# Kernel optimization log

Measured on AMD Instinct MI355X. Metric: run time of the kernel, lower is better.

Reference implementation:

```python
import jax, jax.numpy as jnp
import numpy as np

INPUT_SIZE = 256
HIDDEN_SIZE = 256
BATCH = 64
SEQ_LEN = 2048


def setup_inputs() -> dict:
    key = jax.random.key(0)
    ks = jax.random.split(key, 5)
    s_ih = 1.0 / np.sqrt(HIDDEN_SIZE)
    x = jax.random.normal(ks[0], (BATCH, SEQ_LEN, INPUT_SIZE), dtype=jnp.float32)
    W_ih = jax.random.uniform(ks[1], (4 * HIDDEN_SIZE, INPUT_SIZE), minval=-s_ih, maxval=s_ih, dtype=jnp.float32)
    W_hh = jax.random.uniform(ks[2], (4 * HIDDEN_SIZE, HIDDEN_SIZE), minval=-s_ih, maxval=s_ih, dtype=jnp.float32)
    b_ih = jax.random.uniform(ks[3], (4 * HIDDEN_SIZE,), minval=-s_ih, maxval=s_ih, dtype=jnp.float32)
    b_hh = jax.random.uniform(ks[4], (4 * HIDDEN_SIZE,), minval=-s_ih, maxval=s_ih, dtype=jnp.float32)
    return {"x": x, "W_ih": W_ih, "W_hh": W_hh, "b_ih": b_ih, "b_hh": b_hh}


def _lstm_forward(x, W_ih, W_hh, b_ih, b_hh):
    B, S, _ = x.shape
    H = W_hh.shape[1]
    # Precompute input projections for all timesteps in one big GEMM: [B,S,4H]
    x_proj = jnp.einsum('bsi,gi->bsg', x, W_ih) + b_ih + b_hh

    def step(carry, xp_t):
        h, c = carry
        gates = xp_t + h @ W_hh.T  # [B, 4H]
        i, f, g, o = jnp.split(gates, 4, axis=-1)
        i = jax.nn.sigmoid(i)
        f = jax.nn.sigmoid(f)
        g = jnp.tanh(g)
        o = jax.nn.sigmoid(o)
        c = f * c + i * g
        h = o * jnp.tanh(c)
        return (h, c), h

    h0 = jnp.zeros((B, H), dtype=x.dtype)
    c0 = jnp.zeros((B, H), dtype=x.dtype)
    (h, c), outs = jax.lax.scan(step, (h0, c0), jnp.swapaxes(x_proj, 0, 1))
    outputs = jnp.swapaxes(outs, 0, 1)  # [B, S, H]
    return outputs, (h, c)


def reference(x, W_ih, W_hh, b_ih, b_hh):
    return _lstm_forward(x, W_ih, W_hh, b_ih, b_hh)
```

## Files before the change

### kernel.cpp

```cpp
#include <hip/hip_runtime.h>
#include <hip/hip_bf16.h>

#define BATCH 64
#define SEQ   2048
#define ISZ   256
#define H     256
#define G4    1024
#define M_TOT (BATCH*SEQ)

typedef _Float16 half8  __attribute__((ext_vector_type(8)));
typedef _Float16 half2v __attribute__((ext_vector_type(2)));
typedef float    f32x4  __attribute__((ext_vector_type(4)));

union U32H2 { unsigned int u; half2v h; };
static __device__ __forceinline__ half2v u2h(unsigned int u){ U32H2 x; x.u = u; return x.h; }
union F32I { float f; int i; };

#if __has_builtin(__builtin_amdgcn_fdot2)
#define FDOT2(w,hp,acc) __builtin_amdgcn_fdot2(u2h(w), u2h(hp), (acc), false)
#else
static __device__ __forceinline__ float fdot2_sw(unsigned int w, unsigned int hp, float acc){
  half2v wv = u2h(w), hv = u2h(hp);
  return acc + (float)wv[0]*(float)hv[0] + (float)wv[1]*(float)hv[1];
}
#define FDOT2(w,hp,acc) fdot2_sw((w),(hp),(acc))
#endif

static __device__ __forceinline__ float dpp_xor1(float v){
#if __has_builtin(__builtin_amdgcn_update_dpp)
  F32I a; a.f = v;
  F32I r; r.i = __builtin_amdgcn_update_dpp(0, a.i, 0xB1 , 0xF, 0xF, true);
  return r.f;
#else
  return __shfl_xor(v, 1, 64);
#endif
}
static __device__ __forceinline__ float dpp_xor2(float v){
#if __has_builtin(__builtin_amdgcn_update_dpp)
  F32I a; a.f = v;
  F32I r; r.i = __builtin_amdgcn_update_dpp(0, a.i, 0x4E , 0xF, 0xF, true);
  return r.f;
#else
  return __shfl_xor(v, 2, 64);
#endif
}

__global__ __launch_bounds__(256) void prep_kernel(
    const float* __restrict__ Wih, const float* __restrict__ Whh,
    const float* __restrict__ bih, const float* __restrict__ bhh,
    _Float16* __restrict__ Wihf, unsigned int* __restrict__ Wq,
    float* __restrict__ bias) {
  const int idx = blockIdx.x * 256 + threadIdx.x;
  Wihf[idx] = (_Float16)Wih[idx];
  if (idx < 131072) {
    const int t = idx & 1023, j = idx >> 10;
    const int r = j >> 5, i = j & 31;
    const int row = 4*(t >> 2) + r;
    const int k2  = (t & 3)*32 + i;
    U32H2 p;
    p.h[0] = (_Float16)Whh[row*256 + 2*k2];
    p.h[1] = (_Float16)Whh[row*256 + 2*k2 + 1];
    Wq[idx] = p.u;
  }
  if (idx < 1024) bias[idx] = bih[idx] + bhh[idx];
}

#define BM 128
#define BN 128
#define BK 32
#define LDA 40

__global__ __launch_bounds__(256) void xproj_gemm(
    const float* __restrict__ X, const _Float16* __restrict__ Wihf,
    const float* __restrict__ bias, _Float16* __restrict__ XP) {
  __shared__ _Float16 As[BM*LDA];
  __shared__ _Float16 Bs[BN*LDA];
  const int tid  = threadIdx.x;
  const int m0   = blockIdx.x * BM;
  const int n0   = blockIdx.y * BN;
  const int lane = tid & 63;
  const int w    = tid >> 6;
  const int wm   = w & 1, wn = w >> 1;
  const int row  = tid >> 1, hlf = tid & 1;

  f32x4 acc[4][4];
  #pragma unroll
  for (int mi = 0; mi < 4; ++mi)
    #pragma unroll
    for (int ni = 0; ni < 4; ++ni)
      acc[mi][ni] = (f32x4){0.f, 0.f, 0.f, 0.f};

  for (int kt = 0; kt < ISZ/BK; ++kt) {
    const int k0 = kt * BK;
    __syncthreads();
    {
      const float4* pa = (const float4*)(X + (size_t)(m0+row)*ISZ + k0 + hlf*16);
      float4 f0 = pa[0], f1 = pa[1], f2 = pa[2], f3 = pa[3];
      half8 h0, h1;
      h0[0]=(_Float16)f0.x; h0[1]=(_Float16)f0.y; h0[2]=(_Float16)f0.z; h0[3]=(_Float16)f0.w;
      h0[4]=(_Float16)f1.x; h0[5]=(_Float16)f1.y; h0[6]=(_Float16)f1.z; h0[7]=(_Float16)f1.w;
      h1[0]=(_Float16)f2.x; h1[1]=(_Float16)f2.y; h1[2]=(_Float16)f2.z; h1[3]=(_Float16)f2.w;
      h1[4]=(_Float16)f3.x; h1[5]=(_Float16)f3.y; h1[6]=(_Float16)f3.z; h1[7]=(_Float16)f3.w;
      *(half8*)&As[row*LDA + hlf*16]     = h0;
      *(half8*)&As[row*LDA + hlf*16 + 8] = h1;
      const half8* pb = (const half8*)(Wihf + (size_t)(n0+row)*ISZ + k0 + hlf*16);
      half8 b0 = pb[0], b1 = pb[1];
      *(half8*)&Bs[row*LDA + hlf*16]     = b0;
      *(half8*)&Bs[row*LDA + hlf*16 + 8] = b1;
    }
    __syncthreads();
    const int kch = (lane >> 4) * 8;
    const int rm  = wm*64 + (lane & 15);
    const int rn  = wn*64 + (lane & 15);
    half8 af[4], bf[4];
    #pragma unroll
    for (int i = 0; i < 4; ++i) {
      af[i] = *(const half8*)&As[(rm + i*16)*LDA + kch];
      bf[i] = *(const half8*)&Bs[(rn + i*16)*LDA + kch];
    }
    #pragma unroll
    for (int mi = 0; mi < 4; ++mi)
      #pragma unroll
      for (int ni = 0; ni < 4; ++ni)
        acc[mi][ni] = __builtin_amdgcn_mfma_f32_16x16x32_f16(af[mi], bf[ni], acc[mi][ni], 0, 0, 0);
  }
  const int col = lane & 15, qr = (lane >> 4) * 4;
  #pragma unroll
  for (int ni = 0; ni < 4; ++ni) {
    const int n  = n0 + wn*64 + ni*16 + col;
    const float bs = bias[n];
    #pragma unroll
    for (int mi = 0; mi < 4; ++mi) {
      #pragma unroll
      for (int r = 0; r < 4; ++r) {
        const int m = m0 + wm*64 + mi*16 + qr + r;
        XP[(size_t)m*G4 + n] = (_Float16)(acc[mi][ni][r] + bs);
      }
    }
  }
}

__global__ __launch_bounds__(1024, 4) void lstm_scan(
    const _Float16* __restrict__ XP, const unsigned int* __restrict__ Wq,
    float* __restrict__ out) {
  __shared__ uint4 wlds[8*1024];
  __shared__ float act[G4];
  __shared__ __align__(16) unsigned int h2[144];
  const int t = threadIdx.x;
  const int b = blockIdx.x;

  unsigned int wreg[96];
  #pragma unroll
  for (int j = 0; j < 96; ++j) wreg[j] = Wq[j*1024 + t];
  #pragma unroll
  for (int j = 0; j < 96; ++j) asm volatile("" : "+v"(wreg[j]));

  #pragma unroll
  for (int c = 0; c < 8; ++c) {
    uint4 v;
    v.x = Wq[(96 + 4*c + 0)*1024 + t];
    v.y = Wq[(96 + 4*c + 1)*1024 + t];
    v.z = Wq[(96 + 4*c + 2)*1024 + t];
    v.w = Wq[(96 + 4*c + 3)*1024 + t];
    wlds[c*1024 + t] = v;
  }
  if (t < 144) h2[t] = 0u;
  float c_state = 0.f;
  const _Float16* xb = XP + (size_t)b*SEQ*G4 + t;
  float xcur = (float)xb[0];
  float* outb = out + (size_t)b*SEQ*H;
  const unsigned int* hq_base = h2 + (t & 3)*36;
  __syncthreads();

  #pragma unroll 1
  for (int s = 0; s < SEQ; ++s) {
    const int sn = (s + 1 < SEQ) ? (s + 1) : s;
    const _Float16 xnext = xb[(size_t)sn * G4];

    float a0 = 0.f, a1 = 0.f, a2 = 0.f, a3 = 0.f;
    #pragma unroll
    for (int c = 0; c < 8; ++c) {
      const uint4 hq = *(const uint4*)(hq_base + 4*c);
      a0 = FDOT2(wreg[ 0 + 4*c + 0], hq.x, a0);
      a0 = FDOT2(wreg[ 0 + 4*c + 1], hq.y, a0);
      a0 = FDOT2(wreg[ 0 + 4*c + 2], hq.z, a0);
      a0 = FDOT2(wreg[ 0 + 4*c + 3], hq.w, a0);
      a1 = FDOT2(wreg[32 + 4*c + 0], hq.x, a1);
      a1 = FDOT2(wreg[32 + 4*c + 1], hq.y, a1);
      a1 = FDOT2(wreg[32 + 4*c + 2], hq.z, a1);
      a1 = FDOT2(wreg[32 + 4*c + 3], hq.w, a1);
      a2 = FDOT2(wreg[64 + 4*c + 0], hq.x, a2);
      a2 = FDOT2(wreg[64 + 4*c + 1], hq.y, a2);
      a2 = FDOT2(wreg[64 + 4*c + 2], hq.z, a2);
      a2 = FDOT2(wreg[64 + 4*c + 3], hq.w, a2);
      const uint4 wv = wlds[c*1024 + t];
      a3 = FDOT2(wv.x, hq.x, a3);
      a3 = FDOT2(wv.y, hq.y, a3);
      a3 = FDOT2(wv.z, hq.z, a3);
      a3 = FDOT2(wv.w, hq.w, a3);
    }
    float s0 = a0 + dpp_xor1(a0); s0 += dpp_xor2(s0);
    float s1 = a1 + dpp_xor1(a1); s1 += dpp_xor2(s1);
    float s2 = a2 + dpp_xor1(a2); s2 += dpp_xor2(s2);
    float s3 = a3 + dpp_xor1(a3); s3 += dpp_xor2(s3);
    const int c4 = t & 3;
    const float glo  = (c4 & 1) ? s1 : s0;
    const float ghi  = (c4 & 1) ? s3 : s2;
    const float gate = ((c4 & 2) ? ghi : glo) + xcur;

    float a;
    if (t < 512 || t >= 768) a = 1.f / (1.f + __expf(-gate));
    else                     a = 2.f / (1.f + __expf(-2.f*gate)) - 1.f;
    act[t] = a;
    __syncthreads();
    if (t < H) {
      const float gi = act[t], gf = act[H+t], gg = act[2*H+t], go = act[3*H+t];
      c_state = gf*c_state + gi*gg;
      const float th = 2.f / (1.f + __expf(-2.f*c_state)) - 1.f;
      const float h = go*th;
      outb[(size_t)s*H + t] = h;
      ((_Float16*)h2)[(t >> 6)*72 + (t & 63)] = (_Float16)h;
      if (s == SEQ-1) {
        out[(size_t)BATCH*SEQ*H + (size_t)b*H + t] = h;
        out[(size_t)BATCH*SEQ*H + (size_t)BATCH*H + (size_t)b*H + t] = c_state;
      }
    }
    xcur = (float)xnext;
    __syncthreads();
  }
}

extern "C" void kernel_launch(void* const* d_in, const int* in_sizes, int n_in,
                              void* d_out, int out_size, void* d_ws, size_t ws_size,
                              hipStream_t stream) {
  const float* x   = (const float*)d_in[0];
  const float* Wih = (const float*)d_in[1];
  const float* Whh = (const float*)d_in[2];
  const float* bih = (const float*)d_in[3];
  const float* bhh = (const float*)d_in[4];
  float* out = (float*)d_out;

  char* ws = (char*)d_ws;
  const size_t XP_BYTES = (size_t)M_TOT * G4 * sizeof(_Float16);
  _Float16*     XPp  = (_Float16*)ws;
  _Float16*     Wihf = (_Float16*)(ws + XP_BYTES);
  unsigned int* Wq   = (unsigned int*)(ws + XP_BYTES + 524288);
  float*        bias = (float*)(ws + XP_BYTES + 1048576);

  prep_kernel<<<dim3(1024),            dim3(256),  0, stream>>>(Wih, Whh, bih, bhh, Wihf, Wq, bias);
  xproj_gemm <<<dim3(M_TOT/BM, G4/BN), dim3(256),  0, stream>>>(x, Wihf, bias, XPp);
  lstm_scan  <<<dim3(BATCH),           dim3(1024), 0, stream>>>(XPp, Wq, out);
}
```

Before: 3.755 ms.

## Interleave gate rows per hidden unit and double-buffer h to halve barriers

Permutes the recurrent weight layout so the four gates of one hidden unit sit in four adjacent lanes. The cell update can then gather i/f/g/o with DPP swizzles instead of going through a shared activation array. The h vector is double-buffered in LDS, so each timestep needs one __syncthreads instead of two. A unified sigmoid/tanh formula removes the divergent branch. The cost is that the cell state is computed redundantly in 4 lanes, and the x-projection reads are strided.

```diff
diff --git a/kernel.cpp b/kernel.cpp
--- a/kernel.cpp
+++ b/kernel.cpp
@@ -54,9 +54,9 @@
   Wihf[idx] = (_Float16)Wih[idx];
   if (idx < 131072) {
     const int t = idx & 1023, j = idx >> 10;
-    const int r = j >> 5, i = j & 31;
-    const int row = 4*(t >> 2) + r;
-    const int k2  = (t & 3)*32 + i;
+    const int r_ = j >> 5, i_ = j & 31;
+    const int row = 256*r_ + (t >> 2);
+    const int k2  = (t & 3)*32 + i_;
     U32H2 p;
     p.h[0] = (_Float16)Whh[row*256 + 2*k2];
     p.h[1] = (_Float16)Whh[row*256 + 2*k2 + 1];
@@ -140,14 +140,16 @@
   }
 }
 
-__global__ __launch_bounds__(1024, 4) void lstm_scan(
+__global__ __launch_bounds__(1024)
+__attribute__((amdgpu_waves_per_eu(4, 4)))
+void lstm_scan(
     const _Float16* __restrict__ XP, const unsigned int* __restrict__ Wq,
     float* __restrict__ out) {
   __shared__ uint4 wlds[8*1024];
-  __shared__ float act[G4];
-  __shared__ __align__(16) unsigned int h2[144];
+  __shared__ __align__(16) unsigned int h2[2*144];
   const int t = threadIdx.x;
   const int b = blockIdx.x;
+  const int qd = t >> 2, r = t & 3;
 
   unsigned int wreg[96];
   #pragma unroll
@@ -164,23 +166,29 @@
     v.w = Wq[(96 + 4*c + 3)*1024 + t];
     wlds[c*1024 + t] = v;
   }
-  if (t < 144) h2[t] = 0u;
+  if (t < 2*144) h2[t] = 0u;
+
   float c_state = 0.f;
-  const _Float16* xb = XP + (size_t)b*SEQ*G4 + t;
+  const _Float16* xb = XP + (size_t)b*SEQ*G4 + 256*r + qd;
   float xcur = (float)xb[0];
   float* outb = out + (size_t)b*SEQ*H;
-  const unsigned int* hq_base = h2 + (t & 3)*36;
-  __syncthreads();
+  const unsigned int* hq0 = h2 +       r*36;
+  const unsigned int* hq1 = h2 + 144 + r*36;
+  const int wslot = (qd >> 6)*72 + (qd & 63);
+  const float sc = (r == 2) ? 2.f : 1.f;
+  const float om = (r == 2) ? 1.f : 0.f;
 
   #pragma unroll 1
   for (int s = 0; s < SEQ; ++s) {
+    __syncthreads();
     const int sn = (s + 1 < SEQ) ? (s + 1) : s;
     const _Float16 xnext = xb[(size_t)sn * G4];
 
+    const unsigned int* hb = (s & 1) ? hq1 : hq0;
     float a0 = 0.f, a1 = 0.f, a2 = 0.f, a3 = 0.f;
     #pragma unroll
     for (int c = 0; c < 8; ++c) {
-      const uint4 hq = *(const uint4*)(hq_base + 4*c);
+      const uint4 hq = *(const uint4*)(hb + 4*c);
       a0 = FDOT2(wreg[ 0 + 4*c + 0], hq.x, a0);
       a0 = FDOT2(wreg[ 0 + 4*c + 1], hq.y, a0);
       a0 = FDOT2(wreg[ 0 + 4*c + 2], hq.z, a0);
@@ -203,30 +211,27 @@
     float s1 = a1 + dpp_xor1(a1); s1 += dpp_xor2(s1);
     float s2 = a2 + dpp_xor1(a2); s2 += dpp_xor2(s2);
     float s3 = a3 + dpp_xor1(a3); s3 += dpp_xor2(s3);
-    const int c4 = t & 3;
-    const float glo  = (c4 & 1) ? s1 : s0;
-    const float ghi  = (c4 & 1) ? s3 : s2;
-    const float gate = ((c4 & 2) ? ghi : glo) + xcur;
-
-    float a;
-    if (t < 512 || t >= 768) a = 1.f / (1.f + __expf(-gate));
-    else                     a = 2.f / (1.f + __expf(-2.f*gate)) - 1.f;
-    act[t] = a;
-    __syncthreads();
-    if (t < H) {
-      const float gi = act[t], gf = act[H+t], gg = act[2*H+t], go = act[3*H+t];
-      c_state = gf*c_state + gi*gg;
-      const float th = 2.f / (1.f + __expf(-2.f*c_state)) - 1.f;
-      const float h = go*th;
-      outb[(size_t)s*H + t] = h;
-      ((_Float16*)h2)[(t >> 6)*72 + (t & 63)] = (_Float16)h;
+    const float glo  = (r & 1) ? s1 : s0;
+    const float ghi  = (r & 1) ? s3 : s2;
+    const float gate = ((r & 2) ? ghi : glo) + xcur;
+    const float sg  = 1.f / (1.f + __expf(-sc * gate));
+    const float a   = sc * sg - om;
+    const float fv = dpp_xor1(a);
+    const float gv = dpp_xor2(a);
+    const float ov = dpp_xor1(gv);
+    c_state = fv * c_state + a * gv;
+    const float th = 2.f / (1.f + __expf(-2.f * c_state)) - 1.f;
+    const float h  = ov * th;
+    if (r == 0) {
+      outb[(size_t)s*H + qd] = h;
+      _Float16* h2n = (_Float16*)(h2 + ((s & 1) ? 0 : 144));
+      h2n[wslot] = (_Float16)h;
       if (s == SEQ-1) {
-        out[(size_t)BATCH*SEQ*H + (size_t)b*H + t] = h;
-        out[(size_t)BATCH*SEQ*H + (size_t)BATCH*H + (size_t)b*H + t] = c_state;
+        out[(size_t)BATCH*SEQ*H + (size_t)b*H + qd] = h;
+        out[(size_t)BATCH*SEQ*H + (size_t)BATCH*H + (size_t)b*H + qd] = c_state;
       }
     }
     xcur = (float)xnext;
-    __syncthreads();
   }
 }
 
```

Result: slower. 3.884 ms (+3.4%).
